# Performance work log

Hardware: AMD Instinct MI355X
Metric: run time of the kernel (lower is better)

## Reference

```python
import jax, jax.numpy as jnp
import numpy as np

OMEGA = 30.0
GRID = (48, 48, 48)


def setup_inputs() -> dict:
    key = jax.random.key(0)
    ks = jax.random.split(key, 8)
    B, F_, Cin, Cout, D = 2, 256, 128, 16, 3
    h = jax.random.normal(ks[0], (B, F_, Cin), dtype=jnp.float32)
    y = jax.random.normal(ks[1], (B,) + GRID + (D,), dtype=jnp.float32)
    # Linear params stored as (in, out) for x @ W + b
    Wy = jax.random.normal(ks[2], (D, F_), dtype=jnp.float32) / np.sqrt(D)
    by = jnp.zeros((F_,), dtype=jnp.float32)
    Wh = jax.random.normal(ks[3], (Cin, F_), dtype=jnp.float32) / np.sqrt(Cin)
    bh = jnp.zeros((F_,), dtype=jnp.float32)
    Wu = jax.random.normal(ks[4], (F_, Cout), dtype=jnp.float32) / np.sqrt(F_)
    bu = jnp.zeros((Cout,), dtype=jnp.float32)
    return {"h": h, "y": y, "Wy": Wy, "by": by, "Wh": Wh, "bh": bh, "Wu": Wu, "bu": bu}


def reference(h, y, Wy, by, Wh, bh, Wu, bu):
    # Fourier features over spatial coords: (B, x, y, z, F)
    Y = jnp.sin(2.0 * np.pi * OMEGA * (y @ Wy + by))
    # Per-frequency channel mixing of latent h: (B, F, F)
    H = jax.nn.silu(h @ Wh + bh)
    # Contract over spatial frequencies f -> (B, x, y, z, F)
    n_pts = y.shape[1] * y.shape[2] * y.shape[3]
    U = jnp.einsum('bfc,bxyzf->bxyzc', H, Y) / n_pts
    U = jax.nn.silu(U)
    return U @ Wu + bu
```

## Files before the change

### kernel.cpp

```cpp
#include <hip/hip_runtime.h>
#include <cmath>

#define NPTS 110592
#define FDIM 256
#define CIN  128
#define COUT 16
#define MAIN_BLOCKS 1728
#define BLOCKS_PER_BATCH 864

typedef __attribute__((ext_vector_type(8))) short short8;
typedef __attribute__((ext_vector_type(4))) float floatx4;
typedef __attribute__((ext_vector_type(2))) float f32x2;

union S8U { short8 s; unsigned u[4]; };
union FU { float f; unsigned u; };
union F4P { float4 f4; f32x2 p[2]; };

__device__ __forceinline__ unsigned short bf16_rne(float f) {
  union { float f; unsigned u; } v; v.f = f;
  unsigned r = v.u + 0x7FFFu + ((v.u >> 16) & 1u);
  return (unsigned short)(r >> 16);
}

__device__ __forceinline__ f32x2 pk_fma(f32x2 a, f32x2 b, f32x2 c) {
#if __has_builtin(__builtin_elementwise_fma)
  return __builtin_elementwise_fma(a, b, c);
#else
  f32x2 r; r.x = fmaf(a.x, b.x, c.x); r.y = fmaf(a.y, b.y, c.y); return r;
#endif
}

__global__ __launch_bounds__(256) void prep_kernel(
    const float* __restrict__ h, const float* __restrict__ Wh,
    const float* __restrict__ bh, const float* __restrict__ Wu,
    unsigned short* __restrict__ Ghi, unsigned short* __restrict__ Glo) {
  const int b = blockIdx.x >> 8;
  const int f = blockIdx.x & 255;
  const int t = threadIdx.x;
  const float* __restrict__ hrow = h + (b * FDIM + f) * CIN;
  __shared__ float sH[FDIM];
  __shared__ float sPart[16][17];
  float a0 = 0.f, a1 = 0.f, a2 = 0.f, a3 = 0.f;
  for (int i = 0; i < CIN; i += 4) {
    a0 = fmaf(hrow[i + 0], Wh[(i + 0) * FDIM + t], a0);
    a1 = fmaf(hrow[i + 1], Wh[(i + 1) * FDIM + t], a1);
    a2 = fmaf(hrow[i + 2], Wh[(i + 2) * FDIM + t], a2);
    a3 = fmaf(hrow[i + 3], Wh[(i + 3) * FDIM + t], a3);
  }
  float x = (a0 + a1) + (a2 + a3) + bh[t];
  sH[t] = x / (1.0f + expf(-x));
  __syncthreads();
  const int j = t & 15;
  const int grp = t >> 4;
  float g = 0.f;
  for (int c = grp * 16; c < grp * 16 + 16; ++c)
    g = fmaf(sH[c], Wu[c * COUT + j], g);
  sPart[grp][j] = g;
  __syncthreads();
  if (t < 16) {
    float s = 0.f;
    for (int k = 0; k < 16; ++k) s += sPart[k][t];
    s *= 0.5f / (float)NPTS;
    unsigned short hi = bf16_rne(s);
    union { unsigned u; float f; } vh; vh.u = ((unsigned)hi) << 16;
    unsigned short lo = bf16_rne(s - vh.f);
    Ghi[(b * COUT + t) * FDIM + f] = hi;
    Glo[(b * COUT + t) * FDIM + f] = lo;
  }
}

__global__ __launch_bounds__(128, 4) void main_kernel(
    const float* __restrict__ y, const float* __restrict__ Wy,
    const float* __restrict__ by,
    const unsigned short* __restrict__ Ghi, const unsigned short* __restrict__ Glo,
    const float* __restrict__ bu, float* __restrict__ out) {
  __shared__ __attribute__((aligned(16))) float sC0[FDIM];
  __shared__ __attribute__((aligned(16))) float sC1[FDIM];
  __shared__ __attribute__((aligned(16))) float sC2[FDIM];
  __shared__ __attribute__((aligned(16))) float sC3[FDIM];
  __shared__ __attribute__((aligned(16))) unsigned short sGh[COUT][FDIM + 8];
  __shared__ __attribute__((aligned(16))) unsigned short sGl[COUT][FDIM + 8];

  const int t = threadIdx.x;
  const int blk = blockIdx.x;
  const int b = (blk >= BLOCKS_PER_BATCH) ? 1 : 0;

  sC0[t] = 30.0f * Wy[t];           sC0[t + 128] = 30.0f * Wy[t + 128];
  sC1[t] = 30.0f * Wy[FDIM + t];    sC1[t + 128] = 30.0f * Wy[FDIM + t + 128];
  sC2[t] = 30.0f * Wy[2*FDIM + t];  sC2[t + 128] = 30.0f * Wy[2*FDIM + t + 128];
  sC3[t] = 30.0f * by[t];           sC3[t + 128] = 30.0f * by[t + 128];
  {
    const int row = t >> 3;
    const int c0 = (t & 7) * 32;
    const uint4* srcH = (const uint4*)(Ghi + (b * COUT + row) * FDIM + c0);
    const uint4* srcL = (const uint4*)(Glo + (b * COUT + row) * FDIM + c0);
    uint4 h0 = srcH[0], h1 = srcH[1];
    uint4 l0 = srcL[0], l1 = srcL[1];
    *(uint4*)&sGh[row][c0]      = h0;
    *(uint4*)&sGh[row][c0 + 8]  = h1;
    *(uint4*)&sGh[row][c0 + 16] = *(const uint4*)((const char*)srcH + 32);
    *(uint4*)&sGh[row][c0 + 24] = *(const uint4*)((const char*)srcH + 48);
    *(uint4*)&sGl[row][c0]      = l0;
    *(uint4*)&sGl[row][c0 + 8]  = l1;
    *(uint4*)&sGl[row][c0 + 16] = *(const uint4*)((const char*)srcL + 32);
    *(uint4*)&sGl[row][c0 + 24] = *(const uint4*)((const char*)srcL + 48);
  }
  __syncthreads();

  const int lane = t & 63;
  const int wv = t >> 6;
  const int q = lane >> 4;
  const int m = lane & 15;
  const int pbase = blk * 128 + wv * 64;

  float ya[4], yb[4], yc[4];
#pragma unroll
  for (int tau = 0; tau < 4; ++tau) {
    const int P = pbase + tau * 16 + m;
    ya[tau] = y[3 * P + 0];
    yb[tau] = y[3 * P + 1];
    yc[tau] = y[3 * P + 2];
  }

  floatx4 acc[4];
#pragma unroll
  for (int tau = 0; tau < 4; ++tau) acc[tau] = (floatx4){0.f, 0.f, 0.f, 0.f};

#pragma unroll 2
  for (int k0 = 0; k0 < 8; ++k0) {
    const int fb = k0 * 32 + q * 8;
    F4P c0a, c0b, c1a, c1b, c2a, c2b, c3a, c3b;
    c0a.f4 = *(const float4*)&sC0[fb];  c0b.f4 = *(const float4*)&sC0[fb + 4];
    c1a.f4 = *(const float4*)&sC1[fb];  c1b.f4 = *(const float4*)&sC1[fb + 4];
    c2a.f4 = *(const float4*)&sC2[fb];  c2b.f4 = *(const float4*)&sC2[fb + 4];
    c3a.f4 = *(const float4*)&sC3[fb];  c3b.f4 = *(const float4*)&sC3[fb + 4];
    S8U gh, gl;
    gh.s = *(const short8*)&sGh[m][fb];
    gl.s = *(const short8*)&sGl[m][fb];
#pragma unroll
    for (int tau = 0; tau < 4; ++tau) {
      const f32x2 v0 = {ya[tau], ya[tau]};
      const f32x2 v1 = {yb[tau], yb[tau]};
      const f32x2 v2 = {yc[tau], yc[tau]};
      const f32x2 p01 = pk_fma(v0, c0a.p[0], pk_fma(v1, c1a.p[0], pk_fma(v2, c2a.p[0], c3a.p[0])));
      const f32x2 p23 = pk_fma(v0, c0a.p[1], pk_fma(v1, c1a.p[1], pk_fma(v2, c2a.p[1], c3a.p[1])));
      const f32x2 p45 = pk_fma(v0, c0b.p[0], pk_fma(v1, c1b.p[0], pk_fma(v2, c2b.p[0], c3b.p[0])));
      const f32x2 p67 = pk_fma(v0, c0b.p[1], pk_fma(v1, c1b.p[1], pk_fma(v2, c2b.p[1], c3b.p[1])));
      FU r0, r1, r2, r3, r4, r5, r6, r7;
      r0.f = __builtin_amdgcn_sinf(__builtin_amdgcn_fractf(p01.x));
      r1.f = __builtin_amdgcn_sinf(__builtin_amdgcn_fractf(p01.y));
      r2.f = __builtin_amdgcn_sinf(__builtin_amdgcn_fractf(p23.x));
      r3.f = __builtin_amdgcn_sinf(__builtin_amdgcn_fractf(p23.y));
      r4.f = __builtin_amdgcn_sinf(__builtin_amdgcn_fractf(p45.x));
      r5.f = __builtin_amdgcn_sinf(__builtin_amdgcn_fractf(p45.y));
      r6.f = __builtin_amdgcn_sinf(__builtin_amdgcn_fractf(p67.x));
      r7.f = __builtin_amdgcn_sinf(__builtin_amdgcn_fractf(p67.y));
      const unsigned u0 = r0.u + 0x8000u, u1 = r1.u + 0x8000u;
      const unsigned u2 = r2.u + 0x8000u, u3 = r3.u + 0x8000u;
      const unsigned u4 = r4.u + 0x8000u, u5 = r5.u + 0x8000u;
      const unsigned u6 = r6.u + 0x8000u, u7 = r7.u + 0x8000u;
      S8U af;
      af.u[0] = __builtin_amdgcn_perm(u1, u0, 0x07060302u);
      af.u[1] = __builtin_amdgcn_perm(u3, u2, 0x07060302u);
      af.u[2] = __builtin_amdgcn_perm(u5, u4, 0x07060302u);
      af.u[3] = __builtin_amdgcn_perm(u7, u6, 0x07060302u);
      acc[tau] = __builtin_amdgcn_mfma_f32_16x16x32_bf16(af.s, gh.s, acc[tau], 0, 0, 0);
      acc[tau] = __builtin_amdgcn_mfma_f32_16x16x32_bf16(af.s, gl.s, acc[tau], 0, 0, 0);
    }
  }

  const float bv = bu[m];
#pragma unroll
  for (int tau = 0; tau < 4; ++tau) {
#pragma unroll
    for (int r = 0; r < 4; ++r) {
      const int p = pbase + tau * 16 + q * 4 + r;
      out[p * COUT + m] = acc[tau][r] + bv;
    }
  }
}

extern "C" void kernel_launch(void* const* d_in, const int* in_sizes, int n_in,
                              void* d_out, int out_size, void* d_ws, size_t ws_size,
                              hipStream_t stream) {
  const float* h  = (const float*)d_in[0];
  const float* y  = (const float*)d_in[1];
  const float* Wy = (const float*)d_in[2];
  const float* by = (const float*)d_in[3];
  const float* Wh = (const float*)d_in[4];
  const float* bh = (const float*)d_in[5];
  const float* Wu = (const float*)d_in[6];
  const float* bu = (const float*)d_in[7];
  float* out = (float*)d_out;

  unsigned short* Ghi = (unsigned short*)d_ws;
  unsigned short* Glo = Ghi + 2 * COUT * FDIM;

  prep_kernel<<<512, 256, 0, stream>>>(h, Wh, bh, Wu, Ghi, Glo);
  main_kernel<<<MAIN_BLOCKS, 128, 0, stream>>>(y, Wy, by, Ghi, Glo, bu, out);
}
```

Measured before the change: 94.88 us.

## Batch eight frequency rows per prep block and double main kernel block size

The prep kernel now computes eight frequency rows per block with 64 blocks instead of one row per block with 512, so each Wh load is reused across eight rows and block scheduling overhead shrinks. The main kernel moves to 256 threads per block with half as many blocks, which halves how often the Wy and G tables are staged into shared memory per point. The tradeoff is fewer blocks in the prep kernel (64 on a large GPU), which lowers parallelism there, plus larger blocks in the main kernel.

```diff
diff --git a/kernel.cpp b/kernel.cpp
--- a/kernel.cpp
+++ b/kernel.cpp
@@ -5,8 +5,8 @@
 #define FDIM 256
 #define CIN  128
 #define COUT 16
-#define MAIN_BLOCKS 1728
-#define BLOCKS_PER_BATCH 864
+#define MAIN_BLOCKS 864
+#define BLOCKS_PER_BATCH 432
 
 typedef __attribute__((ext_vector_type(8))) short short8;
 typedef __attribute__((ext_vector_type(4))) float floatx4;
@@ -34,42 +34,52 @@
     const float* __restrict__ h, const float* __restrict__ Wh,
     const float* __restrict__ bh, const float* __restrict__ Wu,
     unsigned short* __restrict__ Ghi, unsigned short* __restrict__ Glo) {
-  const int b = blockIdx.x >> 8;
-  const int f = blockIdx.x & 255;
+  const int b = blockIdx.x >> 5;
+  const int fbase = (blockIdx.x & 31) * 8;
   const int t = threadIdx.x;
-  const float* __restrict__ hrow = h + (b * FDIM + f) * CIN;
-  __shared__ float sH[FDIM];
-  __shared__ float sPart[16][17];
-  float a0 = 0.f, a1 = 0.f, a2 = 0.f, a3 = 0.f;
-  for (int i = 0; i < CIN; i += 4) {
-    a0 = fmaf(hrow[i + 0], Wh[(i + 0) * FDIM + t], a0);
-    a1 = fmaf(hrow[i + 1], Wh[(i + 1) * FDIM + t], a1);
-    a2 = fmaf(hrow[i + 2], Wh[(i + 2) * FDIM + t], a2);
-    a3 = fmaf(hrow[i + 3], Wh[(i + 3) * FDIM + t], a3);
-  }
-  float x = (a0 + a1) + (a2 + a3) + bh[t];
-  sH[t] = x / (1.0f + expf(-x));
+  __shared__ float sH[8][FDIM + 1];
+  __shared__ float sPart[8][33];
+
+  const float* __restrict__ hrows = h + (b * FDIM + fbase) * CIN;
+  float acc[8];
+#pragma unroll
+  for (int r = 0; r < 8; ++r) acc[r] = 0.f;
+  for (int i = 0; i < CIN; ++i) {
+    const float wv = Wh[i * FDIM + t];
+#pragma unroll
+    for (int r = 0; r < 8; ++r)
+      acc[r] = fmaf(hrows[r * CIN + i], wv, acc[r]);
+  }
+#pragma unroll
+  for (int r = 0; r < 8; ++r) {
+    const float x = acc[r] + bh[t];
+    sH[r][t] = x / (1.0f + expf(-x));
+  }
   __syncthreads();
-  const int j = t & 15;
-  const int grp = t >> 4;
-  float g = 0.f;
-  for (int c = grp * 16; c < grp * 16 + 16; ++c)
-    g = fmaf(sH[c], Wu[c * COUT + j], g);
-  sPart[grp][j] = g;
+  {
+    const int r = t >> 5;
+    const int rem = t & 31;
+    const int j = rem >> 1;
+    const int half = rem & 1;
+    float g = 0.f;
+    for (int c = half * 128; c < half * 128 + 128; ++c)
+      g = fmaf(sH[r][c], Wu[c * COUT + j], g);
+    sPart[r][rem] = g;
+  }
   __syncthreads();
-  if (t < 16) {
-    float s = 0.f;
-    for (int k = 0; k < 16; ++k) s += sPart[k][t];
-    s *= 0.5f / (float)NPTS;
+  if (t < 128) {
+    const int r = t >> 4;
+    const int j = t & 15;
+    float s = (sPart[r][2 * j] + sPart[r][2 * j + 1]) * (0.5f / (float)NPTS);
     unsigned short hi = bf16_rne(s);
     union { unsigned u; float f; } vh; vh.u = ((unsigned)hi) << 16;
     unsigned short lo = bf16_rne(s - vh.f);
-    Ghi[(b * COUT + t) * FDIM + f] = hi;
-    Glo[(b * COUT + t) * FDIM + f] = lo;
-  }
-}
-
-__global__ __launch_bounds__(128, 4) void main_kernel(
+    Ghi[(b * COUT + j) * FDIM + fbase + r] = hi;
+    Glo[(b * COUT + j) * FDIM + fbase + r] = lo;
+  }
+}
+
+__global__ __launch_bounds__(256, 4) void main_kernel(
     const float* __restrict__ y, const float* __restrict__ Wy,
     const float* __restrict__ by,
     const unsigned short* __restrict__ Ghi, const unsigned short* __restrict__ Glo,
@@ -85,25 +95,21 @@
   const int blk = blockIdx.x;
   const int b = (blk >= BLOCKS_PER_BATCH) ? 1 : 0;
 
-  sC0[t] = 30.0f * Wy[t];           sC0[t + 128] = 30.0f * Wy[t + 128];
-  sC1[t] = 30.0f * Wy[FDIM + t];    sC1[t + 128] = 30.0f * Wy[FDIM + t + 128];
-  sC2[t] = 30.0f * Wy[2*FDIM + t];  sC2[t + 128] = 30.0f * Wy[2*FDIM + t + 128];
-  sC3[t] = 30.0f * by[t];           sC3[t + 128] = 30.0f * by[t + 128];
+  sC0[t] = 30.0f * Wy[t];
+  sC1[t] = 30.0f * Wy[FDIM + t];
+  sC2[t] = 30.0f * Wy[2 * FDIM + t];
+  sC3[t] = 30.0f * by[t];
   {
-    const int row = t >> 3;
-    const int c0 = (t & 7) * 32;
+    const int row = t >> 4;
+    const int c0 = (t & 15) * 16;
     const uint4* srcH = (const uint4*)(Ghi + (b * COUT + row) * FDIM + c0);
     const uint4* srcL = (const uint4*)(Glo + (b * COUT + row) * FDIM + c0);
     uint4 h0 = srcH[0], h1 = srcH[1];
     uint4 l0 = srcL[0], l1 = srcL[1];
-    *(uint4*)&sGh[row][c0]      = h0;
-    *(uint4*)&sGh[row][c0 + 8]  = h1;
-    *(uint4*)&sGh[row][c0 + 16] = *(const uint4*)((const char*)srcH + 32);
-    *(uint4*)&sGh[row][c0 + 24] = *(const uint4*)((const char*)srcH + 48);
-    *(uint4*)&sGl[row][c0]      = l0;
-    *(uint4*)&sGl[row][c0 + 8]  = l1;
-    *(uint4*)&sGl[row][c0 + 16] = *(const uint4*)((const char*)srcL + 32);
-    *(uint4*)&sGl[row][c0 + 24] = *(const uint4*)((const char*)srcL + 48);
+    *(uint4*)&sGh[row][c0]     = h0;
+    *(uint4*)&sGh[row][c0 + 8] = h1;
+    *(uint4*)&sGl[row][c0]     = l0;
+    *(uint4*)&sGl[row][c0 + 8] = l1;
   }
   __syncthreads();
 
@@ -111,7 +117,7 @@
   const int wv = t >> 6;
   const int q = lane >> 4;
   const int m = lane & 15;
-  const int pbase = blk * 128 + wv * 64;
+  const int pbase = blk * 256 + wv * 64;
 
   float ya[4], yb[4], yc[4];
 #pragma unroll
@@ -196,6 +202,6 @@
   unsigned short* Ghi = (unsigned short*)d_ws;
   unsigned short* Glo = Ghi + 2 * COUT * FDIM;
 
-  prep_kernel<<<512, 256, 0, stream>>>(h, Wh, bh, Wu, Ghi, Glo);
-  main_kernel<<<MAIN_BLOCKS, 128, 0, stream>>>(y, Wy, by, Ghi, Glo, bu, out);
-}
+  prep_kernel<<<64, 256, 0, stream>>>(h, Wh, bh, Wu, Ghi, Glo);
+  main_kernel<<<MAIN_BLOCKS, 256, 0, stream>>>(y, Wy, by, Ghi, Glo, bu, out);
+}
```

Result: slower. 108.4 us (+14.2%).
